# Performance work log

Hardware: AMD Instinct MI355X
Metric: run time of the kernel (lower is better)

Reference implementation:

```python
import jax, jax.numpy as jnp
import numpy as np

GAMMA = 1.0  # RBF kernel width (init kwarg gamma)
N_PAIRS = 8_388_608
N_LAYERS = 8


def setup_inputs() -> dict:
    key = jax.random.key(0)
    ks = jax.random.split(key, 12)
    inp = {
        "x": jax.random.normal(ks[0], (N_PAIRS, 2), dtype=jnp.float32),
        "y": jax.random.normal(ks[1], (N_PAIRS, 2), dtype=jnp.float32),
        # input layer (clip=False)
        "W0": jax.random.normal(ks[2], (2, 2), dtype=jnp.float32),
        "b0": jax.random.normal(ks[3], (2,), dtype=jnp.float32),
        "scale0": jax.random.uniform(ks[4], (2,), dtype=jnp.float32),
        "shift0": jax.random.normal(ks[5], (2,), dtype=jnp.float32),
        # hidden layers (weights/biases clipped to [-5, 5] at construction)
        "Ws": jnp.clip(jax.random.normal(ks[6], (N_LAYERS, 2, 2), dtype=jnp.float32), -5.0, 5.0),
        "bs": jnp.clip(jax.random.normal(ks[7], (N_LAYERS, 2), dtype=jnp.float32), -5.0, 5.0),
        "scales": jax.random.uniform(ks[8], (N_LAYERS, 2), dtype=jnp.float32),
        "shifts": jax.random.normal(ks[9], (N_LAYERS, 2), dtype=jnp.float32),
        # final head Linear(2, 1)
        "Wf": jax.random.normal(ks[10], (1, 2), dtype=jnp.float32),
        "bf": jax.random.normal(ks[11], (1,), dtype=jnp.float32),
    }
    return inp


def _fraud_net(z, W0, b0, scale0, shift0, Ws, bs, scales, shifts, Wf, bf):
    # input layer: tanh(Linear(2,2)) * scale + shift   (z: [N,2])
    z = jnp.tanh(z @ W0.T + b0) * scale0 + shift0

    def step(z, p):
        W, b, s, t = p
        return jnp.tanh(z @ W.T + b) * s + t, None

    z, _ = jax.lax.scan(step, z, (Ws, bs, scales, shifts))
    # final Linear(2, 1) then squeeze -> [N]
    return (z @ Wf.T + bf)[..., 0]


def reference(x, y, W0, b0, scale0, shift0, Ws, bs, scales, shifts, Wf, bf):
    diff = x - y  # [N, 2]
    rbf = jnp.exp(-GAMMA * jnp.sum(diff * diff, axis=-1))  # [N]
    fx = _fraud_net(x, W0, b0, scale0, shift0, Ws, bs, scales, shifts, Wf, bf)
    fy = _fraud_net(y, W0, b0, scale0, shift0, Ws, bs, scales, shifts, Wf, bf)
    return rbf * fx * fy  # [N]
```

## Files before the change

kernel.cpp:

```cpp
#include <hip/hip_runtime.h>
#include <math.h>

#define N_LAYERS 8
#define TAB 48
#define TABSZ (TAB * TAB)
#define LOG2E2 2.8853900817779268f
#define NLOG2E 1.4426950408889634f
#define UCLAMP 24.0f

#if __has_builtin(__builtin_amdgcn_exp2f)
__device__ __forceinline__ float exp2_fast(float x) { return __builtin_amdgcn_exp2f(x); }
#else
__device__ __forceinline__ float exp2_fast(float x) { return __expf(0.6931471805599453f * x); }
#endif

__global__ void setup_meta(const float* __restrict__ W0, const float* __restrict__ b0,
                           const float* __restrict__ s0, const float* __restrict__ t0,
                           float* __restrict__ fp) {
    if (threadIdx.x == 0 && blockIdx.x == 0) {
        fp[0] = LOG2E2 * W0[0]; fp[1] = LOG2E2 * W0[1];
        fp[2] = LOG2E2 * W0[2]; fp[3] = LOG2E2 * W0[3];
        fp[4] = LOG2E2 * b0[0]; fp[5] = LOG2E2 * b0[1];
        for (int c = 0; c < 2; ++c) {
            float s = s0[c], t = t0[c];
            float span = fmaxf(2.2f * s, 1e-5f);
            float h  = span / (float)(TAB - 1);
            float lo = t - 0.5f * span;
            float ih = (float)(TAB - 1) / span;
            fp[6 + c]  = (s + 0.5f * span) * ih;
            fp[8 + c]  = 2.0f * s * ih;
            fp[10 + c] = lo;
            fp[12 + c] = h;
        }
    }
}

__global__ void build_table(const float* __restrict__ Ws, const float* __restrict__ bs,
                            const float* __restrict__ ss, const float* __restrict__ ts,
                            const float* __restrict__ Wf, const float* __restrict__ bf,
                            const float* __restrict__ fp, float* __restrict__ gt) {
    int idx = blockIdx.x * 256 + threadIdx.x;
    if (idx >= TABSZ) return;
    int k1 = idx / TAB, k0 = idx - k1 * TAB;
    float z0 = fp[10] + (float)k0 * fp[12];
    float z1 = fp[11] + (float)k1 * fp[13];
    for (int l = 0; l < N_LAYERS; ++l) {
        float u0 = fmaf(z0, Ws[4 * l + 0], fmaf(z1, Ws[4 * l + 1], bs[2 * l + 0]));
        float u1 = fmaf(z0, Ws[4 * l + 2], fmaf(z1, Ws[4 * l + 3], bs[2 * l + 1]));
        z0 = fmaf(tanhf(u0), ss[2 * l + 0], ts[2 * l + 0]);
        z1 = fmaf(tanhf(u1), ss[2 * l + 1], ts[2 * l + 1]);
    }
    gt[idx] = fmaf(z0, Wf[0], fmaf(z1, Wf[1], bf[0]));
}

__global__ void pack_table(const float* __restrict__ gt, float4* __restrict__ gt4) {
    int idx = blockIdx.x * 256 + threadIdx.x;
    if (idx >= TABSZ) return;
    int iy = idx / TAB, ix = idx - iy * TAB;
    const float* row = gt + iy * TAB;
    int c0 = max(ix - 1, 0);
    int c1 = ix;
    int c2 = min(ix + 1, TAB - 1);
    int c3 = min(ix + 2, TAB - 1);
    gt4[idx] = make_float4(row[c0], row[c1], row[c2], row[c3]);
}

__device__ __forceinline__ void cr_w(float f, float w[4]) {
    w[0] = f * fmaf(f, fmaf(f, -0.5f, 1.0f), -0.5f);
    w[1] = fmaf(f * f, fmaf(f, 1.5f, -2.5f), 1.0f);
    w[2] = f * fmaf(f, fmaf(f, -1.5f, 2.0f), 0.5f);
    w[3] = f * f * fmaf(f, 0.5f, -0.5f);
}

__device__ __forceinline__ float interp_two(const float4* __restrict__ tab4,
                                            float ax0, float ax1, float ay0, float ay1) {
    int ixa = min(max((int)ax0, 1), TAB - 3);
    int iya = min(max((int)ax1, 1), TAB - 3);
    int ixb = min(max((int)ay0, 1), TAB - 3);
    int iyb = min(max((int)ay1, 1), TAB - 3);
    float fxa = ax0 - (float)ixa, fya = ax1 - (float)iya;
    float fxb = ay0 - (float)ixb, fyb = ay1 - (float)iyb;

    const float4* pa = tab4 + (iya - 1) * TAB + ixa;
    const float4* pb = tab4 + (iyb - 1) * TAB + ixb;
    float4 a0 = pa[0], a1 = pa[TAB], a2 = pa[2 * TAB], a3 = pa[3 * TAB];
    float4 b0 = pb[0], b1 = pb[TAB], b2 = pb[2 * TAB], b3 = pb[3 * TAB];

    float wxa[4], wya[4], wxb[4], wyb[4];
    cr_w(fxa, wxa); cr_w(fya, wya);
    cr_w(fxb, wxb); cr_w(fyb, wyb);

    float ra0 = fmaf(a0.w, wxa[3], fmaf(a0.z, wxa[2], fmaf(a0.y, wxa[1], a0.x * wxa[0])));
    float ra1 = fmaf(a1.w, wxa[3], fmaf(a1.z, wxa[2], fmaf(a1.y, wxa[1], a1.x * wxa[0])));
    float ra2 = fmaf(a2.w, wxa[3], fmaf(a2.z, wxa[2], fmaf(a2.y, wxa[1], a2.x * wxa[0])));
    float ra3 = fmaf(a3.w, wxa[3], fmaf(a3.z, wxa[2], fmaf(a3.y, wxa[1], a3.x * wxa[0])));
    float gx  = fmaf(ra3, wya[3], fmaf(ra2, wya[2], fmaf(ra1, wya[1], ra0 * wya[0])));

    float rb0 = fmaf(b0.w, wxb[3], fmaf(b0.z, wxb[2], fmaf(b0.y, wxb[1], b0.x * wxb[0])));
    float rb1 = fmaf(b1.w, wxb[3], fmaf(b1.z, wxb[2], fmaf(b1.y, wxb[1], b1.x * wxb[0])));
    float rb2 = fmaf(b2.w, wxb[3], fmaf(b2.z, wxb[2], fmaf(b2.y, wxb[1], b2.x * wxb[0])));
    float rb3 = fmaf(b3.w, wxb[3], fmaf(b3.z, wxb[2], fmaf(b3.y, wxb[1], b3.x * wxb[0])));
    float gy  = fmaf(rb3, wyb[3], fmaf(rb2, wyb[2], fmaf(rb1, wyb[1], rb0 * wyb[0])));

    return gx * gy;
}

__device__ __forceinline__ float pair_val(const float4* __restrict__ tab4,
                                          float px0, float px1, float py0, float py1,
                                          float C0, float C1, float D0, float D1) {
    float d0 = exp2_fast(fminf(px0, UCLAMP)) + 1.0f;
    float d1 = exp2_fast(fminf(px1, UCLAMP)) + 1.0f;
    float d2 = exp2_fast(fminf(py0, UCLAMP)) + 1.0f;
    float d3 = exp2_fast(fminf(py1, UCLAMP)) + 1.0f;
    float p2 = d0 * d1, p3 = p2 * d2, p4 = p3 * d3;
    float R = __builtin_amdgcn_rcpf(p4);
    float i3 = R * p3;  R *= d3;
    float i2 = R * p2;  R *= d2;
    float i1 = R * d0;
    float i0 = R * d1;
    float ux0 = fmaf(-D0, i0, C0), ux1 = fmaf(-D1, i1, C1);
    float uy0 = fmaf(-D0, i2, C0), uy1 = fmaf(-D1, i3, C1);
    return interp_two(tab4, ux0, ux1, uy0, uy1);
}

__global__ __launch_bounds__(256) void fraud_kernel(
    const float4* __restrict__ x4, const float4* __restrict__ y4,
    const float* __restrict__ fp, const float4* __restrict__ gt4,
    float2* __restrict__ out2, int stride)
{
    __shared__ float4 tab4[TABSZ];
    for (int j = threadIdx.x; j < TABSZ; j += 256) tab4[j] = gt4[j];
    __syncthreads();

    float Wt0 = fp[0], Wt1 = fp[1], Wt2 = fp[2], Wt3 = fp[3];
    float bt0 = fp[4], bt1 = fp[5];
    float C0 = fp[6], C1 = fp[7], D0 = fp[8], D1 = fp[9];

    int tid = blockIdx.x * 256 + threadIdx.x;
#pragma unroll
    for (int k = 0; k < 4; ++k) {
        int g = tid + k * stride;
        float4 xa = x4[g], ya = y4[g];

        float pxa0 = fmaf(xa.x, Wt0, fmaf(xa.y, Wt1, bt0));
        float pxa1 = fmaf(xa.x, Wt2, fmaf(xa.y, Wt3, bt1));
        float pya0 = fmaf(ya.x, Wt0, fmaf(ya.y, Wt1, bt0));
        float pya1 = fmaf(ya.x, Wt2, fmaf(ya.y, Wt3, bt1));
        float dxA = xa.x - ya.x, dyA = xa.y - ya.y;
        float rA = exp2_fast(-NLOG2E * fmaf(dxA, dxA, dyA * dyA));
        float resA = rA * pair_val(tab4, pxa0, pxa1, pya0, pya1, C0, C1, D0, D1);

        float pxb0 = fmaf(xa.z, Wt0, fmaf(xa.w, Wt1, bt0));
        float pxb1 = fmaf(xa.z, Wt2, fmaf(xa.w, Wt3, bt1));
        float pyb0 = fmaf(ya.z, Wt0, fmaf(ya.w, Wt1, bt0));
        float pyb1 = fmaf(ya.z, Wt2, fmaf(ya.w, Wt3, bt1));
        float dxB = xa.z - ya.z, dyB = xa.w - ya.w;
        float rB = exp2_fast(-NLOG2E * fmaf(dxB, dxB, dyB * dyB));
        float resB = rB * pair_val(tab4, pxb0, pxb1, pyb0, pyb1, C0, C1, D0, D1);

        out2[g] = make_float2(resA, resB);
    }
}

extern "C" void kernel_launch(void* const* d_in, const int* in_sizes, int n_in,
                              void* d_out, int out_size, void* d_ws, size_t ws_size,
                              hipStream_t stream) {
    const float* x  = (const float*)d_in[0];
    const float* y  = (const float*)d_in[1];
    const float* W0 = (const float*)d_in[2];
    const float* b0 = (const float*)d_in[3];
    const float* s0 = (const float*)d_in[4];
    const float* t0 = (const float*)d_in[5];
    const float* Ws = (const float*)d_in[6];
    const float* bs = (const float*)d_in[7];
    const float* ss = (const float*)d_in[8];
    const float* ts = (const float*)d_in[9];
    const float* Wf = (const float*)d_in[10];
    const float* bf = (const float*)d_in[11];
    float* out = (float*)d_out;
    float* fp  = (float*)d_ws;
    float* gt  = fp + 16;
    float4* gt4 = (float4*)(fp + 16 + TABSZ);

    hipLaunchKernelGGL(setup_meta, dim3(1), dim3(64), 0, stream, W0, b0, s0, t0, fp);
    hipLaunchKernelGGL(build_table, dim3((TABSZ + 255) / 256), dim3(256), 0, stream,
                       Ws, bs, ss, ts, Wf, bf, fp, gt);
    hipLaunchKernelGGL(pack_table, dim3((TABSZ + 255) / 256), dim3(256), 0, stream,
                       gt, gt4);

    int n       = out_size;
    int ngroups = n / 2;
    int threads = ngroups / 4;
    dim3 block(256);
    dim3 grid(threads / 256);
    hipLaunchKernelGGL(fraud_kernel, grid, block, 0, stream,
                       (const float4*)x, (const float4*)y, fp, gt4,
                       (float2*)out, threads);
}
```

Before: 192.9 us.

## Fuse table setup kernels into one launch and use 512-thread main blocks

```diff
diff --git a/kernel.cpp b/kernel.cpp
--- a/kernel.cpp
+++ b/kernel.cpp
@@ -7,6 +7,7 @@
 #define LOG2E2 2.8853900817779268f
 #define NLOG2E 1.4426950408889634f
 #define UCLAMP 24.0f
+#define BLK 512
 
 #if __has_builtin(__builtin_amdgcn_exp2f)
 __device__ __forceinline__ float exp2_fast(float x) { return __builtin_amdgcn_exp2f(x); }
@@ -14,55 +15,59 @@
 __device__ __forceinline__ float exp2_fast(float x) { return __expf(0.6931471805599453f * x); }
 #endif
 
-__global__ void setup_meta(const float* __restrict__ W0, const float* __restrict__ b0,
-                           const float* __restrict__ s0, const float* __restrict__ t0,
-                           float* __restrict__ fp) {
-    if (threadIdx.x == 0 && blockIdx.x == 0) {
-        fp[0] = LOG2E2 * W0[0]; fp[1] = LOG2E2 * W0[1];
-        fp[2] = LOG2E2 * W0[2]; fp[3] = LOG2E2 * W0[3];
-        fp[4] = LOG2E2 * b0[0]; fp[5] = LOG2E2 * b0[1];
+
+__global__ __launch_bounds__(1024) void setup_all(
+    const float* __restrict__ W0, const float* __restrict__ b0,
+    const float* __restrict__ s0, const float* __restrict__ t0,
+    const float* __restrict__ Ws, const float* __restrict__ bs,
+    const float* __restrict__ ss, const float* __restrict__ ts,
+    const float* __restrict__ Wf, const float* __restrict__ bf,
+    float* __restrict__ fp, float4* __restrict__ gt4) {
+    __shared__ float gs[TABSZ];
+    __shared__ float fs[16];
+
+    if (threadIdx.x == 0) {
+        fs[0] = LOG2E2 * W0[0]; fs[1] = LOG2E2 * W0[1];
+        fs[2] = LOG2E2 * W0[2]; fs[3] = LOG2E2 * W0[3];
+        fs[4] = LOG2E2 * b0[0]; fs[5] = LOG2E2 * b0[1];
         for (int c = 0; c < 2; ++c) {
             float s = s0[c], t = t0[c];
             float span = fmaxf(2.2f * s, 1e-5f);
             float h  = span / (float)(TAB - 1);
             float lo = t - 0.5f * span;
             float ih = (float)(TAB - 1) / span;
-            fp[6 + c]  = (s + 0.5f * span) * ih;
-            fp[8 + c]  = 2.0f * s * ih;
-            fp[10 + c] = lo;
-            fp[12 + c] = h;
+            fs[6 + c]  = (s + 0.5f * span) * ih;
+            fs[8 + c]  = 2.0f * s * ih;
+            fs[10 + c] = lo;
+            fs[12 + c] = h;
         }
-    }
-}
-
-__global__ void build_table(const float* __restrict__ Ws, const float* __restrict__ bs,
-                            const float* __restrict__ ss, const float* __restrict__ ts,
-                            const float* __restrict__ Wf, const float* __restrict__ bf,
-                            const float* __restrict__ fp, float* __restrict__ gt) {
-    int idx = blockIdx.x * 256 + threadIdx.x;
-    if (idx >= TABSZ) return;
-    int k1 = idx / TAB, k0 = idx - k1 * TAB;
-    float z0 = fp[10] + (float)k0 * fp[12];
-    float z1 = fp[11] + (float)k1 * fp[13];
-    for (int l = 0; l < N_LAYERS; ++l) {
-        float u0 = fmaf(z0, Ws[4 * l + 0], fmaf(z1, Ws[4 * l + 1], bs[2 * l + 0]));
-        float u1 = fmaf(z0, Ws[4 * l + 2], fmaf(z1, Ws[4 * l + 3], bs[2 * l + 1]));
-        z0 = fmaf(tanhf(u0), ss[2 * l + 0], ts[2 * l + 0]);
-        z1 = fmaf(tanhf(u1), ss[2 * l + 1], ts[2 * l + 1]);
-    }
-    gt[idx] = fmaf(z0, Wf[0], fmaf(z1, Wf[1], bf[0]));
-}
-
-__global__ void pack_table(const float* __restrict__ gt, float4* __restrict__ gt4) {
-    int idx = blockIdx.x * 256 + threadIdx.x;
-    if (idx >= TABSZ) return;
-    int iy = idx / TAB, ix = idx - iy * TAB;
-    const float* row = gt + iy * TAB;
-    int c0 = max(ix - 1, 0);
-    int c1 = ix;
-    int c2 = min(ix + 1, TAB - 1);
-    int c3 = min(ix + 2, TAB - 1);
-    gt4[idx] = make_float4(row[c0], row[c1], row[c2], row[c3]);
+        for (int i = 0; i < 14; ++i) fp[i] = fs[i];
+    }
+    __syncthreads();
+
+    for (int idx = threadIdx.x; idx < TABSZ; idx += blockDim.x) {
+        int k1 = idx / TAB, k0 = idx - k1 * TAB;
+        float z0 = fs[10] + (float)k0 * fs[12];
+        float z1 = fs[11] + (float)k1 * fs[13];
+        for (int l = 0; l < N_LAYERS; ++l) {
+            float u0 = fmaf(z0, Ws[4 * l + 0], fmaf(z1, Ws[4 * l + 1], bs[2 * l + 0]));
+            float u1 = fmaf(z0, Ws[4 * l + 2], fmaf(z1, Ws[4 * l + 3], bs[2 * l + 1]));
+            z0 = fmaf(tanhf(u0), ss[2 * l + 0], ts[2 * l + 0]);
+            z1 = fmaf(tanhf(u1), ss[2 * l + 1], ts[2 * l + 1]);
+        }
+        gs[idx] = fmaf(z0, Wf[0], fmaf(z1, Wf[1], bf[0]));
+    }
+    __syncthreads();
+
+    for (int idx = threadIdx.x; idx < TABSZ; idx += blockDim.x) {
+        int iy = idx / TAB, ix = idx - iy * TAB;
+        const float* row = gs + iy * TAB;
+        int c0 = max(ix - 1, 0);
+        int c1 = ix;
+        int c2 = min(ix + 1, TAB - 1);
+        int c3 = min(ix + 2, TAB - 1);
+        gt4[idx] = make_float4(row[c0], row[c1], row[c2], row[c3]);
+    }
 }
 
 __device__ __forceinline__ void cr_w(float f, float w[4]) {
@@ -123,20 +128,20 @@
     return interp_two(tab4, ux0, ux1, uy0, uy1);
 }
 
-__global__ __launch_bounds__(256) void fraud_kernel(
+__global__ __launch_bounds__(BLK, 8) void fraud_kernel(
     const float4* __restrict__ x4, const float4* __restrict__ y4,
     const float* __restrict__ fp, const float4* __restrict__ gt4,
     float2* __restrict__ out2, int stride)
 {
     __shared__ float4 tab4[TABSZ];
-    for (int j = threadIdx.x; j < TABSZ; j += 256) tab4[j] = gt4[j];
+    for (int j = threadIdx.x; j < TABSZ; j += BLK) tab4[j] = gt4[j];
     __syncthreads();
 
     float Wt0 = fp[0], Wt1 = fp[1], Wt2 = fp[2], Wt3 = fp[3];
     float bt0 = fp[4], bt1 = fp[5];
     float C0 = fp[6], C1 = fp[7], D0 = fp[8], D1 = fp[9];
 
-    int tid = blockIdx.x * 256 + threadIdx.x;
+    int tid = blockIdx.x * BLK + threadIdx.x;
 #pragma unroll
     for (int k = 0; k < 4; ++k) {
         int g = tid + k * stride;
@@ -179,20 +184,16 @@
     const float* bf = (const float*)d_in[11];
     float* out = (float*)d_out;
     float* fp  = (float*)d_ws;
-    float* gt  = fp + 16;
-    float4* gt4 = (float4*)(fp + 16 + TABSZ);
-
-    hipLaunchKernelGGL(setup_meta, dim3(1), dim3(64), 0, stream, W0, b0, s0, t0, fp);
-    hipLaunchKernelGGL(build_table, dim3((TABSZ + 255) / 256), dim3(256), 0, stream,
-                       Ws, bs, ss, ts, Wf, bf, fp, gt);
-    hipLaunchKernelGGL(pack_table, dim3((TABSZ + 255) / 256), dim3(256), 0, stream,
-                       gt, gt4);
+    float4* gt4 = (float4*)(fp + 16);
+
+    hipLaunchKernelGGL(setup_all, dim3(1), dim3(1024), 0, stream,
+                       W0, b0, s0, t0, Ws, bs, ss, ts, Wf, bf, fp, gt4);
 
     int n       = out_size;
     int ngroups = n / 2;
     int threads = ngroups / 4;
-    dim3 block(256);
-    dim3 grid(threads / 256);
+    dim3 block(BLK);
+    dim3 grid(threads / BLK);
     hipLaunchKernelGGL(fraud_kernel, grid, block, 0, stream,
                        (const float4*)x, (const float4*)y, fp, gt4,
                        (float2*)out, threads);
```

Result: faster. 186.2 us (-3.5%).
